# Kernel tuning notes

Measured on AMD Instinct MI355X. Metric: run time of the kernel, lower is better.

Reference implementation:

```python
import jax, jax.numpy as jnp
import numpy as np

B, S, H, TOK = 64, 512, 768, 8   # batch rows, tokens/row, hidden, tokens per sentence
K = (B * S) // TOK               # 4096 sentence segments
NUM_CLASSES = 4


def setup_inputs() -> dict:
    key = jax.random.key(0)
    k0, k1, k2, k3 = jax.random.split(key, 4)
    out = jax.random.normal(k0, (B, S, H), dtype=jnp.float32)
    # each row i holds sentences i*64 .. i*64+63, 8 contiguous tokens each
    sent_ids = (jnp.arange(B * S, dtype=jnp.int64) // TOK).reshape(B, S)
    labels = jax.random.randint(k1, (B, S), 0, NUM_CLASSES, dtype=jnp.int64)
    W1 = jax.random.normal(k2, (2 * H, 512), dtype=jnp.float32) * 0.02
    b1 = jnp.zeros((512,), dtype=jnp.float32)
    W2 = jax.random.normal(k3, (512, NUM_CLASSES), dtype=jnp.float32) * 0.02
    b2 = jnp.zeros((NUM_CLASSES,), dtype=jnp.float32)
    return {"out": out, "W1": W1, "b1": b1, "W2": W2, "b2": b2,
            "labels": labels, "sent_ids": sent_ids}


def _ner_forward(out, W1, b1, W2, b2, labels, sent_ids):
    ids = sent_ids.reshape(-1)                      # [B*S]
    x = out.reshape(-1, H)                          # [B*S, H]
    n = ids.shape[0]
    valid = ids >= 0                                # -1 means padding
    seg = jnp.where(valid, ids, K).astype(jnp.int32)  # route invalid to dummy slot K
    w = valid.astype(out.dtype)

    # masked segment mean of token embeddings (avg_vector)
    counts = jax.ops.segment_sum(w, seg, num_segments=K + 1)[:K]            # [K]
    sums = jax.ops.segment_sum(x * w[:, None], seg, num_segments=K + 1)[:K]  # [K,H]
    seg_mean = sums / jnp.maximum(counts, 1.0)[:, None]

    # build_dict: cls vector of segment k = out[i][0] of LAST row containing k
    row = jnp.arange(n) // S
    cls_row = jax.ops.segment_max(jnp.where(valid, row, -1), seg, num_segments=K + 1)[:K]
    cls_vec = out[jnp.maximum(cls_row, 0), 0]       # [K, H]

    # segment label = labels[mask][0] (first token in flattened order)
    first_idx = jax.ops.segment_min(jnp.where(valid, jnp.arange(n), n), seg,
                                    num_segments=K + 1)[:K]
    seg_label = labels.reshape(-1)[jnp.minimum(first_idx, n - 1)]  # [K]

    feats = jnp.concatenate([cls_vec, seg_mean], axis=1)  # [K, 2H]
    h = jax.nn.relu(feats @ W1 + b1)                      # dropout is identity in eval
    probs = jax.nn.softmax(h @ W2 + b2, axis=1)           # [K, 4]

    # Multiclass_Focal_Loss: gather prob at label, -log, sorted truncated sum
    p = jnp.take_along_axis(probs, seg_label[:, None].astype(jnp.int32), axis=1)[:, 0]
    costs = -jnp.log(p)                                   # [K]
    pos = seg_label > 0
    Npos = jnp.sum(pos)
    neg_costs = jnp.where(seg_label == 0, costs, -jnp.inf)
    sorted_desc = -jnp.sort(-neg_costs)                   # descending
    M = jnp.floor(2.5 * Npos.astype(jnp.float32)).astype(jnp.int32)
    take = (jnp.arange(K) < M) & jnp.isfinite(sorted_desc)
    total = jnp.sum(jnp.where(pos, costs, 0.0)) + jnp.sum(jnp.where(take, sorted_desc, 0.0))
    denom = jnp.floor(3.5 * Npos.astype(jnp.float32))
    return total / denom


def reference(out, W1, b1, W2, b2, labels, sent_ids):
    return _ner_forward(out, W1, b1, W2, b2, labels, sent_ids)
```

## Files before the change

kernel.cpp:

```cpp
#include <hip/hip_runtime.h>
#include <hip/hip_bf16.h>
#include <math.h>

#define SDIM 512
#define HDIM 768
#define TOKN 8
#define KSEG 4096
#define HID 512
#define NCLS 4
#define NPANEL 16

typedef __attribute__((ext_vector_type(8))) short short8v;
typedef __attribute__((ext_vector_type(4))) float f32x4;

__device__ __forceinline__ ushort f2bf(float f) {
    union { float f; unsigned u; } x; x.f = f;
    return (ushort)((x.u + 0x7FFFu + ((x.u >> 16) & 1u)) >> 16);
}

__global__ __launch_bounds__(192) void seg_mean_k(const float* __restrict__ outp,
                                                  float* __restrict__ segm) {
    int k = blockIdx.x;
    int c = threadIdx.x;
    const float4* base = (const float4*)(outp + (size_t)k * TOKN * HDIM) + c;
    float x = 0.f, y = 0.f, z = 0.f, w = 0.f;
#pragma unroll
    for (int t = 0; t < TOKN; ++t) {
        float4 v = base[t * (HDIM / 4)];
        x += v.x; y += v.y; z += v.z; w += v.w;
    }
    float4 m = make_float4(x * 0.125f, y * 0.125f, z * 0.125f, w * 0.125f);
    ((float4*)(segm + (size_t)k * HDIM))[c] = m;
}

__global__ __launch_bounds__(256) void prep_small_k(const float* __restrict__ outp,
                                                    const float* __restrict__ W1,
                                                    ushort* __restrict__ W1t,
                                                    float* __restrict__ clsW,
                                                    float* __restrict__ gaccf,
                                                    unsigned* __restrict__ gcnt) {
    __shared__ __align__(16) char smem[18432];
    int bid = blockIdx.x, tid = threadIdx.x;

    if (bid < 8) {
        ushort (*As)[72] = (ushort(*)[72])smem;
        ushort (*Bs)[72] = (ushort(*)[72])(smem + 9216);
        if (bid == 0) {
            if (tid < 2) gaccf[tid] = 0.f;
            if (tid < 3) gcnt[tid] = 0u;
        }
        int nc = bid * 64;
        int lane = tid & 63, wid = tid >> 6;
        int wm = wid >> 1, wn = wid & 1;
        f32x4 acc[2][2] = {};
        int am = tid >> 2, aq = tid & 3;
        int bk = tid >> 4, bq = tid & 15;
        for (int kt = 0; kt < HDIM; kt += 64) {
#pragma unroll
            for (int i = 0; i < 4; ++i) {
                int k = aq * 16 + i * 4;
                float4 v = *(const float4*)(outp + (size_t)am * SDIM * HDIM + kt + k);
                ushort4 u;
                u.x = f2bf(v.x); u.y = f2bf(v.y); u.z = f2bf(v.z); u.w = f2bf(v.w);
                *(ushort4*)(&As[am][k]) = u;
            }
#pragma unroll
            for (int i = 0; i < 4; ++i) {
                int krow = bk + i * 16;
                int n4 = bq * 4;
                float4 v = *(const float4*)(W1 + (size_t)(kt + krow) * HID + nc + n4);
                Bs[n4 + 0][krow] = f2bf(v.x);
                Bs[n4 + 1][krow] = f2bf(v.y);
                Bs[n4 + 2][krow] = f2bf(v.z);
                Bs[n4 + 3][krow] = f2bf(v.w);
            }
            __syncthreads();
            int row = lane & 15, kc = lane >> 4;
#pragma unroll
            for (int ks = 0; ks < 2; ++ks) {
                int kk = ks * 32 + kc * 8;
                short8v afrag[2], bfrag[2];
#pragma unroll
                for (int f = 0; f < 2; ++f) {
                    afrag[f] = *(const short8v*)(&As[wm * 32 + f * 16 + row][kk]);
                    bfrag[f] = *(const short8v*)(&Bs[wn * 32 + f * 16 + row][kk]);
                }
#pragma unroll
                for (int mf = 0; mf < 2; ++mf)
#pragma unroll
                    for (int nf = 0; nf < 2; ++nf)
                        acc[mf][nf] = __builtin_amdgcn_mfma_f32_16x16x32_bf16(
                            afrag[mf], bfrag[nf], acc[mf][nf], 0, 0, 0);
            }
            __syncthreads();
        }
        int col = lane & 15, rg = lane >> 4;
#pragma unroll
        for (int mf = 0; mf < 2; ++mf)
#pragma unroll
            for (int nf = 0; nf < 2; ++nf) {
                int gn = nc + wn * 32 + nf * 16 + col;
#pragma unroll
                for (int r = 0; r < 4; ++r) {
                    int gm = wm * 32 + mf * 16 + rg * 4 + r;
                    clsW[gm * HID + gn] = acc[mf][nf][r];
                }
            }
    } else {
        float (*tile)[33] = (float(*)[33])smem;
        int idx = bid - 8;
        int k0 = (idx % 24) * 32;
        int n0 = (idx / 24) * 32;
        int tx = tid & 31, ty = tid >> 5;
#pragma unroll
        for (int i = 0; i < 4; ++i) {
            int kl = ty + i * 8;
            tile[kl][tx] = W1[(size_t)(HDIM + k0 + kl) * HID + n0 + tx];
        }
        __syncthreads();
#pragma unroll
        for (int i = 0; i < 4; ++i) {
            int nl = ty + i * 8;
            W1t[(size_t)(n0 + nl) * HDIM + k0 + tx] = f2bf(tile[tx][nl]);
        }
    }
}

#define BM 64
#define BN 64
#define BKK 64

__global__ __launch_bounds__(256) void gemm_head_k(const float* __restrict__ A,
                                                   const ushort* __restrict__ Bt,
                                                   const float* __restrict__ clsW,
                                                   const float* __restrict__ b1,
                                                   const float* __restrict__ W2,
                                                   float* __restrict__ plog) {
    __shared__ ushort As[BM][72];
    __shared__ ushort Bs[BN][72];

    int tid = threadIdx.x, lane = tid & 63, wid = tid >> 6;
    int wm = wid >> 1, wn = wid & 1;
    int m0 = blockIdx.x * BM, n0 = blockIdx.y * BN;
    int ar = tid >> 2, ac = tid & 3;
    int br = tid >> 3, bc = tid & 7;

    f32x4 acc[2][2] = {};
    float4 pa[4], pb[2];

#pragma unroll
    for (int i = 0; i < 4; ++i)
        pa[i] = *(const float4*)(A + (size_t)(m0 + ar) * HDIM + ac * 16 + i * 4);
#pragma unroll
    for (int i = 0; i < 2; ++i)
        pb[i] = *(const float4*)(Bt + (size_t)(n0 + br + 32 * i) * HDIM + bc * 8);

    for (int kt = 0; kt < HDIM; kt += BKK) {
#pragma unroll
        for (int i = 0; i < 4; ++i) {
            ushort4 u;
            u.x = f2bf(pa[i].x); u.y = f2bf(pa[i].y);
            u.z = f2bf(pa[i].z); u.w = f2bf(pa[i].w);
            *(ushort4*)(&As[ar][ac * 16 + i * 4]) = u;
        }
#pragma unroll
        for (int i = 0; i < 2; ++i)
            *(float4*)(&Bs[br + 32 * i][bc * 8]) = pb[i];
        __syncthreads();
        int nkt = kt + BKK;
        if (nkt < HDIM) {
#pragma unroll
            for (int i = 0; i < 4; ++i)
                pa[i] = *(const float4*)(A + (size_t)(m0 + ar) * HDIM + nkt + ac * 16 + i * 4);
#pragma unroll
            for (int i = 0; i < 2; ++i)
                pb[i] = *(const float4*)(Bt + (size_t)(n0 + br + 32 * i) * HDIM + nkt + bc * 8);
        }
        int row = lane & 15, kc = lane >> 4;
#pragma unroll
        for (int ks = 0; ks < 2; ++ks) {
            int kk = ks * 32 + kc * 8;
            short8v afrag[2], bfrag[2];
#pragma unroll
            for (int f = 0; f < 2; ++f) {
                afrag[f] = *(const short8v*)(&As[wm * 32 + f * 16 + row][kk]);
                bfrag[f] = *(const short8v*)(&Bs[wn * 32 + f * 16 + row][kk]);
            }
#pragma unroll
            for (int mf = 0; mf < 2; ++mf)
#pragma unroll
                for (int nf = 0; nf < 2; ++nf)
                    acc[mf][nf] = __builtin_amdgcn_mfma_f32_16x16x32_bf16(
                        afrag[mf], bfrag[nf], acc[mf][nf], 0, 0, 0);
        }
        __syncthreads();
    }

    int col = lane & 15, rg = lane >> 4;
    float4 w2v[2];
#pragma unroll
    for (int nf = 0; nf < 2; ++nf) {
        int gn = n0 + wn * 32 + nf * 16 + col;
        float bb = b1[gn];
        float cw = clsW[blockIdx.x * HID + gn];
        w2v[nf] = *(const float4*)(W2 + gn * 4);
#pragma unroll
        for (int mf = 0; mf < 2; ++mf)
#pragma unroll
            for (int r = 0; r < 4; ++r)
                acc[mf][nf][r] = fmaxf(acc[mf][nf][r] + cw + bb, 0.f);
    }
    int panel = blockIdx.y * 2 + wn;
#pragma unroll
    for (int c = 0; c < NCLS; ++c) {
        float w0 = (c == 0) ? w2v[0].x : (c == 1) ? w2v[0].y : (c == 2) ? w2v[0].z : w2v[0].w;
        float w1 = (c == 0) ? w2v[1].x : (c == 1) ? w2v[1].y : (c == 2) ? w2v[1].z : w2v[1].w;
        float p[2][4];
#pragma unroll
        for (int mf = 0; mf < 2; ++mf)
#pragma unroll
            for (int r = 0; r < 4; ++r)
                p[mf][r] = fmaf(acc[mf][0][r], w0, acc[mf][1][r] * w1);
#pragma unroll
        for (int off = 1; off < 16; off <<= 1)
#pragma unroll
            for (int mf = 0; mf < 2; ++mf)
#pragma unroll
                for (int r = 0; r < 4; ++r)
                    p[mf][r] += __shfl_xor(p[mf][r], off);
        if (col == 0) {
#pragma unroll
            for (int mf = 0; mf < 2; ++mf)
#pragma unroll
                for (int r = 0; r < 4; ++r) {
                    int gm = m0 + wm * 32 + mf * 16 + rg * 4 + r;
                    plog[((size_t)panel * KSEG + gm) * NCLS + c] = p[mf][r];
                }
        }
    }
}

__global__ __launch_bounds__(256) void loss_k(const float* __restrict__ plog,
                                              const float* __restrict__ b2,
                                              const int* __restrict__ labels,
                                              float* __restrict__ gaccf,
                                              unsigned* __restrict__ gcnt,
                                              float* __restrict__ negs,
                                              float* __restrict__ res) {
    __shared__ float s_p[4], s_n[4];
    __shared__ unsigned s_pc[4], s_nc[4];
    __shared__ int s_last;
    int tid = threadIdx.x, bid = blockIdx.x;
    int lane = tid & 63, wid = tid >> 6;
    float b20 = b2[0], b21 = b2[1], b22 = b2[2], b23 = b2[3];

    float psum = 0.f, nsum = 0.f;
    unsigned pcnt = 0, ncnt = 0;
#pragma unroll
    for (int i = 0; i < 2; ++i) {
        int k = bid * 512 + i * 256 + tid;
        float l0 = b20, l1 = b21, l2 = b22, l3 = b23;
#pragma unroll
        for (int pn = 0; pn < NPANEL; ++pn) {
            float4 v = *(const float4*)(plog + ((size_t)pn * KSEG + k) * NCLS);
            l0 += v.x; l1 += v.y; l2 += v.z; l3 += v.w;
        }
        int lb = labels[k * TOKN];
        float mx = fmaxf(fmaxf(l0, l1), fmaxf(l2, l3));
        float se = expf(l0 - mx) + expf(l1 - mx) + expf(l2 - mx) + expf(l3 - mx);
        float ll = (lb == 0) ? l0 : (lb == 1) ? l1 : (lb == 2) ? l2 : l3;
        float ck = logf(se) + mx - ll;
        if (lb > 0) { psum += ck; pcnt++; } else { nsum += ck; ncnt++; }
    }
#pragma unroll
    for (int off = 32; off; off >>= 1) {
        psum += __shfl_down(psum, off);
        nsum += __shfl_down(nsum, off);
        pcnt += __shfl_down(pcnt, off);
        ncnt += __shfl_down(ncnt, off);
    }
    if (lane == 0) { s_p[wid] = psum; s_n[wid] = nsum; s_pc[wid] = pcnt; s_nc[wid] = ncnt; }
    __syncthreads();
    if (tid == 0) {
        float bp = s_p[0] + s_p[1] + s_p[2] + s_p[3];
        float bn = s_n[0] + s_n[1] + s_n[2] + s_n[3];
        unsigned bpc = s_pc[0] + s_pc[1] + s_pc[2] + s_pc[3];
        unsigned bnc = s_nc[0] + s_nc[1] + s_nc[2] + s_nc[3];
        atomicAdd(&gaccf[0], bp);
        atomicAdd(&gaccf[1], bn);
        atomicAdd(&gcnt[0], bpc);
        atomicAdd(&gcnt[1], bnc);
    }
    __threadfence();
    if (tid == 0) {
        unsigned t = atomicAdd(&gcnt[2], 1u);
        s_last = (t == 7) ? 1 : 0;
    }
    __syncthreads();
    if (!s_last) return;
    __threadfence();

    float tp = __hip_atomic_load(&gaccf[0], __ATOMIC_RELAXED, __HIP_MEMORY_SCOPE_AGENT);
    float tn = __hip_atomic_load(&gaccf[1], __ATOMIC_RELAXED, __HIP_MEMORY_SCOPE_AGENT);
    unsigned np = __hip_atomic_load(&gcnt[0], __ATOMIC_RELAXED, __HIP_MEMORY_SCOPE_AGENT);
    unsigned nn = __hip_atomic_load(&gcnt[1], __ATOMIC_RELAXED, __HIP_MEMORY_SCOPE_AGENT);
    int M = (int)floorf(2.5f * (float)np);
    if ((int)nn <= M) {
        if (tid == 0) res[0] = (tp + tn) / floorf(3.5f * (float)np);
        return;
    }

    for (int k = tid; k < KSEG; k += 256) {
        float l0 = b20, l1 = b21, l2 = b22, l3 = b23;
        for (int pn = 0; pn < NPANEL; ++pn) {
            float4 v = *(const float4*)(plog + ((size_t)pn * KSEG + k) * NCLS);
            l0 += v.x; l1 += v.y; l2 += v.z; l3 += v.w;
        }
        int lb = labels[k * TOKN];
        float mx = fmaxf(fmaxf(l0, l1), fmaxf(l2, l3));
        float se = expf(l0 - mx) + expf(l1 - mx) + expf(l2 - mx) + expf(l3 - mx);
        float ll = (lb == 0) ? l0 : (lb == 1) ? l1 : (lb == 2) ? l2 : l3;
        float ck = logf(se) + mx - ll;
        negs[k] = (lb == 0) ? ck : -INFINITY;
    }
    __syncthreads();
    for (int kk = 2; kk <= KSEG; kk <<= 1) {
        for (int j = kk >> 1; j > 0; j >>= 1) {
            for (int i = tid; i < KSEG; i += 256) {
                int ixj = i ^ j;
                if (ixj > i) {
                    float a = negs[i], b = negs[ixj];
                    bool up = ((i & kk) == 0);
                    if (up ? (a > b) : (a < b)) { negs[i] = b; negs[ixj] = a; }
                }
            }
            __syncthreads();
        }
    }
    int M2 = (int)floorf(2.5f * (float)np);
    float s = 0.f;
    for (int i = tid; i < M2; i += 256) {
        float v = negs[KSEG - 1 - i];
        if (isfinite(v)) s += v;
    }
#pragma unroll
    for (int off = 32; off; off >>= 1) s += __shfl_down(s, off);
    if (lane == 0) s_p[wid] = s;
    __syncthreads();
    if (tid == 0) {
        float t = s_p[0] + s_p[1] + s_p[2] + s_p[3];
        res[0] = (tp + t) / floorf(3.5f * (float)np);
    }
}

extern "C" void kernel_launch(void* const* d_in, const int* in_sizes, int n_in,
                              void* d_out, int out_size, void* d_ws, size_t ws_size,
                              hipStream_t stream) {
    const float* outp   = (const float*)d_in[0];
    const float* W1     = (const float*)d_in[1];
    const float* b1     = (const float*)d_in[2];
    const float* W2     = (const float*)d_in[3];
    const float* b2     = (const float*)d_in[4];
    const int*   labels = (const int*)d_in[5];

    char* ws = (char*)d_ws;
    float*    segm  = (float*) ws;
    ushort*   W1t   = (ushort*)(ws + 12582912);
    float*    clsW  = (float*) (ws + 13369344);
    float*    plog  = (float*) (ws + 13500416);
    float*    negs  = (float*) (ws + 14548992);
    float*    gaccf = (float*) (ws + 14565376);
    unsigned* gcnt  = (unsigned*)(ws + 14565384);
    float*    res   = (float*)d_out;

    seg_mean_k<<<KSEG, 192, 0, stream>>>(outp, segm);
    prep_small_k<<<392, 256, 0, stream>>>(outp, W1, W1t, clsW, gaccf, gcnt);
    gemm_head_k<<<dim3(KSEG / BM, HID / BN), 256, 0, stream>>>(
        segm, W1t, clsW, b1, W2, plog);
    loss_k<<<8, 256, 0, stream>>>(plog, b2, labels, gaccf, gcnt, negs, res);
}
```

Measured before the change: 68.94 us.

## Fuse segment-mean into GEMM head kernel with register-resident A fragments

Removes the separate segment-mean kernel and its fp32 intermediate buffer. The new GEMM kernel computes each block's 16 segment means straight from the input, stores them as bf16 in LDS, and keeps all A fragments in registers. Each wave covers 128 hidden columns, streams W1t directly from global/L2, and writes four partial-logit panels instead of sixteen. This cuts an intermediate write and re-read plus one launch. In exchange there are only 256 blocks, no LDS reuse of B, and heavy per-block L2 traffic for the weights.

```diff
diff --git a/kernel.cpp b/kernel.cpp
--- a/kernel.cpp
+++ b/kernel.cpp
@@ -8,7 +8,7 @@
 #define KSEG 4096
 #define HID 512
 #define NCLS 4
-#define NPANEL 16
+#define NPANEL 4
 
 typedef __attribute__((ext_vector_type(8))) short short8v;
 typedef __attribute__((ext_vector_type(4))) float f32x4;
@@ -16,21 +16,6 @@
 __device__ __forceinline__ ushort f2bf(float f) {
     union { float f; unsigned u; } x; x.f = f;
     return (ushort)((x.u + 0x7FFFu + ((x.u >> 16) & 1u)) >> 16);
-}
-
-__global__ __launch_bounds__(192) void seg_mean_k(const float* __restrict__ outp,
-                                                  float* __restrict__ segm) {
-    int k = blockIdx.x;
-    int c = threadIdx.x;
-    const float4* base = (const float4*)(outp + (size_t)k * TOKN * HDIM) + c;
-    float x = 0.f, y = 0.f, z = 0.f, w = 0.f;
-#pragma unroll
-    for (int t = 0; t < TOKN; ++t) {
-        float4 v = base[t * (HDIM / 4)];
-        x += v.x; y += v.y; z += v.z; w += v.w;
-    }
-    float4 m = make_float4(x * 0.125f, y * 0.125f, z * 0.125f, w * 0.125f);
-    ((float4*)(segm + (size_t)k * HDIM))[c] = m;
 }
 
 __global__ __launch_bounds__(256) void prep_small_k(const float* __restrict__ outp,
@@ -126,116 +111,98 @@
     }
 }
 
-#define BM 64
-#define BN 64
-#define BKK 64
-
-__global__ __launch_bounds__(256) void gemm_head_k(const float* __restrict__ A,
-                                                   const ushort* __restrict__ Bt,
-                                                   const float* __restrict__ clsW,
-                                                   const float* __restrict__ b1,
-                                                   const float* __restrict__ W2,
-                                                   float* __restrict__ plog) {
-    __shared__ ushort As[BM][72];
-    __shared__ ushort Bs[BN][72];
-
-    int tid = threadIdx.x, lane = tid & 63, wid = tid >> 6;
-    int wm = wid >> 1, wn = wid & 1;
-    int m0 = blockIdx.x * BM, n0 = blockIdx.y * BN;
-    int ar = tid >> 2, ac = tid & 3;
-    int br = tid >> 3, bc = tid & 7;
-
-    f32x4 acc[2][2] = {};
-    float4 pa[4], pb[2];
-
-#pragma unroll
-    for (int i = 0; i < 4; ++i)
-        pa[i] = *(const float4*)(A + (size_t)(m0 + ar) * HDIM + ac * 16 + i * 4);
-#pragma unroll
-    for (int i = 0; i < 2; ++i)
-        pb[i] = *(const float4*)(Bt + (size_t)(n0 + br + 32 * i) * HDIM + bc * 8);
-
-    for (int kt = 0; kt < HDIM; kt += BKK) {
-#pragma unroll
-        for (int i = 0; i < 4; ++i) {
+#define APAD 776
+
+__global__ __launch_bounds__(256) void seg_gemm_head_k(const float* __restrict__ outp,
+                                                       const ushort* __restrict__ W1t,
+                                                       const float* __restrict__ clsW,
+                                                       const float* __restrict__ b1,
+                                                       const float* __restrict__ W2,
+                                                       float* __restrict__ plog) {
+    __shared__ ushort Am[16][APAD];
+    int tid = threadIdx.x, bm = blockIdx.x;
+    int lane = tid & 63, wid = tid >> 6;
+
+    {
+        const float4* ob = (const float4*)outp + (size_t)bm * 16 * (TOKN * HDIM / 4);
+#pragma unroll 4
+        for (int i = 0; i < 12; ++i) {
+            int o = tid + i * 256;
+            int s = o / 192, c = o % 192;
+            const float4* base = ob + (size_t)s * (TOKN * HDIM / 4) + c;
+            float x = 0.f, y = 0.f, z = 0.f, w = 0.f;
+#pragma unroll
+            for (int t = 0; t < TOKN; ++t) {
+                float4 v = base[t * (HDIM / 4)];
+                x += v.x; y += v.y; z += v.z; w += v.w;
+            }
             ushort4 u;
-            u.x = f2bf(pa[i].x); u.y = f2bf(pa[i].y);
-            u.z = f2bf(pa[i].z); u.w = f2bf(pa[i].w);
-            *(ushort4*)(&As[ar][ac * 16 + i * 4]) = u;
-        }
-#pragma unroll
-        for (int i = 0; i < 2; ++i)
-            *(float4*)(&Bs[br + 32 * i][bc * 8]) = pb[i];
-        __syncthreads();
-        int nkt = kt + BKK;
-        if (nkt < HDIM) {
-#pragma unroll
-            for (int i = 0; i < 4; ++i)
-                pa[i] = *(const float4*)(A + (size_t)(m0 + ar) * HDIM + nkt + ac * 16 + i * 4);
-#pragma unroll
-            for (int i = 0; i < 2; ++i)
-                pb[i] = *(const float4*)(Bt + (size_t)(n0 + br + 32 * i) * HDIM + nkt + bc * 8);
-        }
-        int row = lane & 15, kc = lane >> 4;
-#pragma unroll
-        for (int ks = 0; ks < 2; ++ks) {
-            int kk = ks * 32 + kc * 8;
-            short8v afrag[2], bfrag[2];
-#pragma unroll
-            for (int f = 0; f < 2; ++f) {
-                afrag[f] = *(const short8v*)(&As[wm * 32 + f * 16 + row][kk]);
-                bfrag[f] = *(const short8v*)(&Bs[wn * 32 + f * 16 + row][kk]);
-            }
-#pragma unroll
-            for (int mf = 0; mf < 2; ++mf)
-#pragma unroll
-                for (int nf = 0; nf < 2; ++nf)
-                    acc[mf][nf] = __builtin_amdgcn_mfma_f32_16x16x32_bf16(
-                        afrag[mf], bfrag[nf], acc[mf][nf], 0, 0, 0);
-        }
-        __syncthreads();
+            u.x = f2bf(x * 0.125f); u.y = f2bf(y * 0.125f);
+            u.z = f2bf(z * 0.125f); u.w = f2bf(w * 0.125f);
+            *(ushort4*)(&Am[s][c * 4]) = u;
+        }
+    }
+    __syncthreads();
+
+    int n0 = wid * 128;
+    int brow = lane & 15, kc = lane >> 4;
+    short8v af[24];
+#pragma unroll
+    for (int kt = 0; kt < 24; ++kt)
+        af[kt] = *(const short8v*)(&Am[brow][kt * 32 + kc * 8]);
+
+    f32x4 acc[8];
+    const ushort* bbase = W1t + (size_t)(n0 + brow) * HDIM + kc * 8;
+#pragma unroll
+    for (int np2 = 0; np2 < 4; ++np2) {
+        const ushort* bp0 = bbase + (size_t)(np2 * 2 + 0) * 16 * HDIM;
+        const ushort* bp1 = bbase + (size_t)(np2 * 2 + 1) * 16 * HDIM;
+        f32x4 a0 = {}, a1 = {};
+#pragma unroll
+        for (int kt = 0; kt < 24; ++kt) {
+            short8v bf0 = *(const short8v*)(bp0 + kt * 32);
+            short8v bf1 = *(const short8v*)(bp1 + kt * 32);
+            a0 = __builtin_amdgcn_mfma_f32_16x16x32_bf16(af[kt], bf0, a0, 0, 0, 0);
+            a1 = __builtin_amdgcn_mfma_f32_16x16x32_bf16(af[kt], bf1, a1, 0, 0, 0);
+        }
+        acc[np2 * 2] = a0; acc[np2 * 2 + 1] = a1;
     }
 
     int col = lane & 15, rg = lane >> 4;
-    float4 w2v[2];
-#pragma unroll
-    for (int nf = 0; nf < 2; ++nf) {
-        int gn = n0 + wn * 32 + nf * 16 + col;
+    int cgrp = (bm >> 2) * HID;
+    float4 w2v[8];
+#pragma unroll
+    for (int nf = 0; nf < 8; ++nf) {
+        int gn = n0 + nf * 16 + col;
         float bb = b1[gn];
-        float cw = clsW[blockIdx.x * HID + gn];
+        float cw = clsW[cgrp + gn];
         w2v[nf] = *(const float4*)(W2 + gn * 4);
 #pragma unroll
-        for (int mf = 0; mf < 2; ++mf)
+        for (int r = 0; r < 4; ++r)
+            acc[nf][r] = fmaxf(acc[nf][r] + cw + bb, 0.f);
+    }
+#pragma unroll
+    for (int c = 0; c < NCLS; ++c) {
+        float pc[4] = {};
+#pragma unroll
+        for (int nf = 0; nf < 8; ++nf) {
+            float wv = (c == 0) ? w2v[nf].x : (c == 1) ? w2v[nf].y
+                     : (c == 2) ? w2v[nf].z : w2v[nf].w;
 #pragma unroll
             for (int r = 0; r < 4; ++r)
-                acc[mf][nf][r] = fmaxf(acc[mf][nf][r] + cw + bb, 0.f);
-    }
-    int panel = blockIdx.y * 2 + wn;
-#pragma unroll
-    for (int c = 0; c < NCLS; ++c) {
-        float w0 = (c == 0) ? w2v[0].x : (c == 1) ? w2v[0].y : (c == 2) ? w2v[0].z : w2v[0].w;
-        float w1 = (c == 0) ? w2v[1].x : (c == 1) ? w2v[1].y : (c == 2) ? w2v[1].z : w2v[1].w;
-        float p[2][4];
-#pragma unroll
-        for (int mf = 0; mf < 2; ++mf)
+                pc[r] = fmaf(acc[nf][r], wv, pc[r]);
+        }
+#pragma unroll
+        for (int off = 1; off < 16; off <<= 1)
 #pragma unroll
             for (int r = 0; r < 4; ++r)
-                p[mf][r] = fmaf(acc[mf][0][r], w0, acc[mf][1][r] * w1);
-#pragma unroll
-        for (int off = 1; off < 16; off <<= 1)
-#pragma unroll
-            for (int mf = 0; mf < 2; ++mf)
-#pragma unroll
-                for (int r = 0; r < 4; ++r)
-                    p[mf][r] += __shfl_xor(p[mf][r], off);
+                pc[r] += __shfl_xor(pc[r], off);
         if (col == 0) {
 #pragma unroll
-            for (int mf = 0; mf < 2; ++mf)
-#pragma unroll
-                for (int r = 0; r < 4; ++r) {
-                    int gm = m0 + wm * 32 + mf * 16 + rg * 4 + r;
-                    plog[((size_t)panel * KSEG + gm) * NCLS + c] = p[mf][r];
-                }
+            for (int r = 0; r < 4; ++r) {
+                int gm = bm * 16 + rg * 4 + r;
+                plog[((size_t)wid * KSEG + gm) * NCLS + c] = pc[r];
+            }
         }
     }
 }
@@ -337,9 +304,8 @@
             __syncthreads();
         }
     }
-    int M2 = (int)floorf(2.5f * (float)np);
     float s = 0.f;
-    for (int i = tid; i < M2; i += 256) {
+    for (int i = tid; i < M; i += 256) {
         float v = negs[KSEG - 1 - i];
         if (isfinite(v)) s += v;
     }
@@ -364,18 +330,15 @@
     const int*   labels = (const int*)d_in[5];
 
     char* ws = (char*)d_ws;
-    float*    segm  = (float*) ws;
-    ushort*   W1t   = (ushort*)(ws + 12582912);
-    float*    clsW  = (float*) (ws + 13369344);
-    float*    plog  = (float*) (ws + 13500416);
-    float*    negs  = (float*) (ws + 14548992);
-    float*    gaccf = (float*) (ws + 14565376);
-    unsigned* gcnt  = (unsigned*)(ws + 14565384);
+    ushort*   W1t   = (ushort*)ws;
+    float*    clsW  = (float*) (ws + 786432);
+    float*    plog  = (float*) (ws + 917504);
+    float*    negs  = (float*) (ws + 1179648);
+    float*    gaccf = (float*) (ws + 1196032);
+    unsigned* gcnt  = (unsigned*)(ws + 1196040);
     float*    res   = (float*)d_out;
 
-    seg_mean_k<<<KSEG, 192, 0, stream>>>(outp, segm);
     prep_small_k<<<392, 256, 0, stream>>>(outp, W1, W1t, clsW, gaccf, gcnt);
-    gemm_head_k<<<dim3(KSEG / BM, HID / BN), 256, 0, stream>>>(
-        segm, W1t, clsW, b1, W2, plog);
+    seg_gemm_head_k<<<256, 256, 0, stream>>>(outp, W1t, clsW, b1, W2, plog);
     loss_k<<<8, 256, 0, stream>>>(plog, b2, labels, gaccf, gcnt, negs, res);
 }
```

Measured after the change: 66.89 us. 1.03x faster.
